# Kernel tuning notes

Measured on AMD Instinct MI355X. Metric: run time of the kernel, lower is better.

Reference implementation:

```python
import jax, jax.numpy as jnp
import numpy as np

B, S, H, D, P = 16, 512, 12, 768, 256
TOP_RATE = 0.1
K = int(round(TOP_RATE * S))  # 51, matches round(self.top_rate * hidden_state.size(1))
LN_EPS = 1e-5


def setup_inputs() -> dict:
    key = jax.random.key(0)
    ks = jax.random.split(key, 6)
    return {
        "hidden_state": jax.random.normal(ks[0], (B, S, D), dtype=jnp.float32),
        "attention": jax.random.normal(ks[1], (B, H, S, S), dtype=jnp.float32),
        "length": S,  # uniform valid length (scalar int)
        # node_trans: Linear(D, P)
        "W_node": jax.random.normal(ks[2], (D, P), dtype=jnp.float32) * 0.02,
        "b_node": jnp.zeros((P,), dtype=jnp.float32),
        # node_eta parameter, initialized to 0 (self.node_eta.data.fill_(0))
        "node_eta": jnp.zeros((1,), dtype=jnp.float32),
        # fc: Linear(P, P)
        "W_fc": jax.random.normal(ks[3], (P, P), dtype=jnp.float32) * 0.02,
        "b_fc": jnp.zeros((P,), dtype=jnp.float32),
        # LayerNorm(P)
        "ln_gamma": jnp.ones((P,), dtype=jnp.float32),
        "ln_beta": jnp.zeros((P,), dtype=jnp.float32),
    }


def reference(hidden_state, attention, W_node, b_node, node_eta, W_fc, b_fc,
              ln_gamma, ln_beta, length):
    # average attention over heads: [B, S, S]
    avg_atten = attention.mean(axis=1)
    # per-target-node top-k neighbors
    vals, idx = jax.lax.top_k(avg_atten, K)  # [B, S, K]
    # edge mask replicating softmax(where(v>0, v, -1e9)) followed by nonzero():
    # entries at -1e9 underflow to exactly 0 in fp32 softmax iff the row has a
    # positive value; otherwise the softmax is uniform and all edges survive.
    keep = vals > 0.0
    row_has_pos = keep.any(axis=-1, keepdims=True)
    keep = jnp.where(row_has_pos, keep, True)            # [B, S, K] (>=1 True per row)
    keepf = keep.astype(hidden_state.dtype)[..., None]   # [B, S, K, 1]

    # node_trans on all nodes: [B, S, P]
    h = hidden_state @ W_node + b_node

    # gather source-node features h[b, idx[b, t, j], :] -> [B, S, K, P]
    gathered = jax.vmap(lambda hb, ib: hb[ib])(h, idx)

    # reduce='mean': edge weight w=1, mailbox mean over kept incoming edges
    h_agg = (gathered * keepf).sum(axis=2) / keepf.sum(axis=2)

    eta = node_eta[0]
    new_h = eta * h + (1.0 - eta) * h_agg                # [B, S, P]

    # dgl.mean_nodes: mean over the `length` nodes of each sub-graph (=S here)
    out = new_h.mean(axis=1)                             # [B, P]

    # fc(dropout(tanh(out))) with dropout in eval mode (identity)
    out = jnp.tanh(out) @ W_fc + b_fc

    # LayerNorm
    mu = out.mean(axis=-1, keepdims=True)
    var = ((out - mu) ** 2).mean(axis=-1, keepdims=True)
    out = (out - mu) / jnp.sqrt(var + LN_EPS) * ln_gamma + ln_beta
    return out
```

## Files before the change

### kernel.cpp

```cpp
#include <hip/hip_runtime.h>
#include <math.h>

#define B_ 16
#define S_ 512
#define H_ 12
#define D_ 768
#define P_ 256
#define K_ 51
#define CH_ 16
#define NCHUNK_ (S_/CH_)

__device__ __forceinline__ unsigned okey(float f) {
  unsigned u = __float_as_uint(f);
  return (u & 0x80000000u) ? ~u : (u | 0x80000000u);
}

__global__ __launch_bounds__(256) void k1_topk_weights(
    const float* __restrict__ attn, float* __restrict__ w) {
  const int bt = blockIdx.x;
  const int b = bt >> 9;
  const int t = bt & (S_ - 1);
  const int tid = threadIdx.x;

  __shared__ unsigned keys[S_];
  __shared__ unsigned hist[256];
  __shared__ unsigned sbuf[256];
  __shared__ int ipar[4];

  const float* base = attn + (((size_t)b * H_) * S_ + t) * S_;
  float2 acc = make_float2(0.f, 0.f);
  #pragma unroll
  for (int h = 0; h < H_; ++h) {
    const float2 v = *(const float2*)(base + (size_t)h * S_ * S_ + 2 * tid);
    acc.x += v.x; acc.y += v.y;
  }
  const float a0 = acc.x * (1.0f / (float)H_);
  const float a1 = acc.y * (1.0f / (float)H_);
  const unsigned k0 = okey(a0);
  const unsigned k1v = okey(a1);
  keys[2 * tid] = k0;
  keys[2 * tid + 1] = k1v;

  if (tid == 0) ipar[0] = 0;
  __syncthreads();
  {
    const int myPos = (a0 > 0.f) + (a1 > 0.f);
    if (myPos) atomicAdd(&ipar[0], myPos);
  }
  __syncthreads();
  const int p = ipar[0];

  bool sel0, sel1;
  float invcnt;
  if (p >= 1 && p < K_) {
    sel0 = (a0 > 0.f);
    sel1 = (a1 > 0.f);
    invcnt = 1.0f / (float)p;
  } else {
    unsigned prefix = 0;
    int remaining = K_;
    #pragma unroll
    for (int pass = 0; pass < 4; ++pass) {
      const int shift = 24 - 8 * pass;
      const unsigned pm = (pass == 0) ? 0u : (0xFFFFFFFFu << (shift + 8));
      hist[tid] = 0;
      __syncthreads();
      if ((k0 & pm) == prefix) atomicAdd(&hist[(k0 >> shift) & 255u], 1u);
      if ((k1v & pm) == prefix) atomicAdd(&hist[(k1v >> shift) & 255u], 1u);
      __syncthreads();
      if (tid < 64) {
        const int lane = tid;
        const unsigned c0 = hist[4 * lane + 0];
        const unsigned c1 = hist[4 * lane + 1];
        const unsigned c2 = hist[4 * lane + 2];
        const unsigned c3 = hist[4 * lane + 3];
        const unsigned loc = c0 + c1 + c2 + c3;
        unsigned suf = loc;
        #pragma unroll
        for (int off = 1; off < 64; off <<= 1) {
          const unsigned v = __shfl_down(suf, off, 64);
          if (lane + off < 64) suf += v;
        }
        const unsigned after = suf - loc;
        sbuf[4 * lane + 3] = after + c3;
        sbuf[4 * lane + 2] = after + c3 + c2;
        sbuf[4 * lane + 1] = after + c3 + c2 + c1;
        sbuf[4 * lane + 0] = after + c3 + c2 + c1 + c0;
      }
      __syncthreads();
      const unsigned sd = sbuf[tid];
      const unsigned sd1 = (tid < 255) ? sbuf[tid + 1] : 0u;
      if (sd >= (unsigned)remaining && sd1 < (unsigned)remaining) {
        ipar[1] = tid;
        ipar[2] = (int)sd1;
        ipar[3] = (int)(sd - sd1);
      }
      __syncthreads();
      prefix |= ((unsigned)ipar[1]) << shift;
      remaining -= ipar[2];
    }
    const unsigned T = prefix;
    const int tieCnt = ipar[3];
    sel0 = (k0 > T);
    sel1 = (k1v > T);
    if (tieCnt == remaining) {
      sel0 |= (k0 == T);
      sel1 |= (k1v == T);
    } else {
      if (k0 == T) {
        int r = 0;
        for (int s2 = 0; s2 < 2 * tid; ++s2) r += (keys[s2] == T);
        if (r < remaining) sel0 = true;
      }
      if (k1v == T) {
        int r = 0;
        for (int s2 = 0; s2 < 2 * tid + 1; ++s2) r += (keys[s2] == T);
        if (r < remaining) sel1 = true;
      }
    }
    invcnt = 1.0f / (float)K_;
  }

  float* wrow = w + b * S_;
  if (sel0) atomicAdd(&wrow[2 * tid], invcnt);
  if (sel1) atomicAdd(&wrow[2 * tid + 1], invcnt);
}

__global__ __launch_bounds__(192) void k2_weighted_sum(
    const float* __restrict__ hidden, const float* __restrict__ w,
    const float* __restrict__ node_eta, float* __restrict__ x) {
  const int chunk = blockIdx.x;
  const int b = blockIdx.y;
  const int tid = threadIdx.x;
  __shared__ float coef[CH_];
  if (tid < CH_) {
    const float eta = node_eta[0];
    const float wv = w[b * S_ + chunk * CH_ + tid];
    coef[tid] = (eta + (1.0f - eta) * wv) * (1.0f / (float)S_);
  }
  __syncthreads();
  const float* hb = hidden + ((size_t)b * S_ + (size_t)chunk * CH_) * D_ + 4 * tid;
  float4 acc = make_float4(0.f, 0.f, 0.f, 0.f);
  #pragma unroll
  for (int s = 0; s < CH_; ++s) {
    const float4 v = *(const float4*)(hb + (size_t)s * D_);
    const float c = coef[s];
    acc.x += c * v.x; acc.y += c * v.y; acc.z += c * v.z; acc.w += c * v.w;
  }
  float* xp = x + b * D_ + 4 * tid;
  atomicAdd(xp + 0, acc.x);
  atomicAdd(xp + 1, acc.y);
  atomicAdd(xp + 2, acc.z);
  atomicAdd(xp + 3, acc.w);
}

__global__ __launch_bounds__(256) void k3_final(
    const float* __restrict__ x, const float* __restrict__ W_node,
    const float* __restrict__ b_node, const float* __restrict__ W_fc,
    const float* __restrict__ b_fc, const float* __restrict__ gamma,
    const float* __restrict__ beta, float* __restrict__ out) {
  const int b = blockIdx.x;
  const int tid = threadIdx.x;
  __shared__ float xs[D_];
  __shared__ float ts[P_];
  __shared__ float red[4];

  for (int d = tid; d < D_; d += 256) xs[d] = x[b * D_ + d];
  __syncthreads();

  float v = b_node[tid];
  for (int d = 0; d < D_; ++d) v += xs[d] * W_node[d * P_ + tid];
  ts[tid] = tanhf(v);
  __syncthreads();

  float o = b_fc[tid];
  for (int q = 0; q < P_; ++q) o += ts[q] * W_fc[q * P_ + tid];

  float s = o;
  #pragma unroll
  for (int off = 32; off > 0; off >>= 1) s += __shfl_down(s, off, 64);
  const int wave = tid >> 6, lane = tid & 63;
  if (lane == 0) red[wave] = s;
  __syncthreads();
  const float mu = (red[0] + red[1] + red[2] + red[3]) * (1.0f / (float)P_);
  __syncthreads();
  const float dv = o - mu;
  float s2 = dv * dv;
  #pragma unroll
  for (int off = 32; off > 0; off >>= 1) s2 += __shfl_down(s2, off, 64);
  if (lane == 0) red[wave] = s2;
  __syncthreads();
  const float var = (red[0] + red[1] + red[2] + red[3]) * (1.0f / (float)P_);
  const float inv = 1.0f / sqrtf(var + 1e-5f);
  out[b * P_ + tid] = dv * inv * gamma[tid] + beta[tid];
}

extern "C" void kernel_launch(void* const* d_in, const int* in_sizes, int n_in,
                              void* d_out, int out_size, void* d_ws, size_t ws_size,
                              hipStream_t stream) {
  (void)in_sizes; (void)n_in; (void)out_size; (void)ws_size;
  const float* hidden   = (const float*)d_in[0];
  const float* attn     = (const float*)d_in[1];
  const float* W_node   = (const float*)d_in[3];
  const float* b_node   = (const float*)d_in[4];
  const float* node_eta = (const float*)d_in[5];
  const float* W_fc     = (const float*)d_in[6];
  const float* b_fc     = (const float*)d_in[7];
  const float* gamma    = (const float*)d_in[8];
  const float* beta     = (const float*)d_in[9];
  float* out = (float*)d_out;

  float* w = (float*)d_ws;
  float* x = w + B_ * S_;
  hipMemsetAsync(d_ws, 0, (size_t)(B_ * S_ + B_ * D_) * sizeof(float), stream);

  k1_topk_weights<<<B_ * S_, 256, 0, stream>>>(attn, w);
  k2_weighted_sum<<<dim3(NCHUNK_, B_), 192, 0, stream>>>(hidden, w, node_eta, x);
  k3_final<<<B_, 256, 0, stream>>>(x, W_node, b_node, W_fc, b_fc, gamma, beta, out);
}
```

Baseline: 362.8 us.

## Streamline radix-select top-k with per-wave histograms, ballot counting, early exit

The radix-select in the top-k kernel now keeps four per-wave histograms, double-buffered so the next pass's clear overlaps the current pass. This removes one barrier per pass and spreads shared-memory atomic contention across waves. The positive-value count uses wave ballots instead of per-thread atomics, the threshold search is folded into the scan wave, and the pass loop exits early once the tie bucket is exactly the remaining count. The final GEMV loops are unrolled. The kernel is likely memory-bound on reading the attention tensor, so the select-path savings may be modest.

```diff
diff --git a/kernel.cpp b/kernel.cpp
--- a/kernel.cpp
+++ b/kernel.cpp
@@ -21,11 +21,14 @@
   const int b = bt >> 9;
   const int t = bt & (S_ - 1);
   const int tid = threadIdx.x;
+  const int wave = tid >> 6;
 
   __shared__ unsigned keys[S_];
-  __shared__ unsigned hist[256];
-  __shared__ unsigned sbuf[256];
+  __shared__ __align__(16) unsigned hist[2][4][256];
   __shared__ int ipar[4];
+
+  ((uint4*)&hist[0][0][0])[tid] = uint4{0u, 0u, 0u, 0u};
+  if (tid == 0) ipar[0] = 0;
 
   const float* base = attn + (((size_t)b * H_) * S_ + t) * S_;
   float2 acc = make_float2(0.f, 0.f);
@@ -41,11 +44,10 @@
   keys[2 * tid] = k0;
   keys[2 * tid + 1] = k1v;
 
-  if (tid == 0) ipar[0] = 0;
-  __syncthreads();
   {
-    const int myPos = (a0 > 0.f) + (a1 > 0.f);
-    if (myPos) atomicAdd(&ipar[0], myPos);
+    const unsigned long long m0 = __ballot(a0 > 0.f);
+    const unsigned long long m1 = __ballot(a1 > 0.f);
+    if ((tid & 63) == 0) atomicAdd(&ipar[0], __popcll(m0) + __popcll(m1));
   }
   __syncthreads();
   const int p = ipar[0];
@@ -59,21 +61,25 @@
   } else {
     unsigned prefix = 0;
     int remaining = K_;
-    #pragma unroll
+    int tieCnt = 0;
+    int exited = 0;
+    unsigned exitm = 0;
     for (int pass = 0; pass < 4; ++pass) {
       const int shift = 24 - 8 * pass;
       const unsigned pm = (pass == 0) ? 0u : (0xFFFFFFFFu << (shift + 8));
-      hist[tid] = 0;
+      const int cur = pass & 1, nxt = cur ^ 1;
+      if ((k0 & pm) == prefix) atomicAdd(&hist[cur][wave][(k0 >> shift) & 255u], 1u);
+      if ((k1v & pm) == prefix) atomicAdd(&hist[cur][wave][(k1v >> shift) & 255u], 1u);
+      ((uint4*)&hist[nxt][0][0])[tid] = uint4{0u, 0u, 0u, 0u};
       __syncthreads();
-      if ((k0 & pm) == prefix) atomicAdd(&hist[(k0 >> shift) & 255u], 1u);
-      if ((k1v & pm) == prefix) atomicAdd(&hist[(k1v >> shift) & 255u], 1u);
-      __syncthreads();
-      if (tid < 64) {
+      if (wave == 0) {
         const int lane = tid;
-        const unsigned c0 = hist[4 * lane + 0];
-        const unsigned c1 = hist[4 * lane + 1];
-        const unsigned c2 = hist[4 * lane + 2];
-        const unsigned c3 = hist[4 * lane + 3];
+        unsigned c0 = 0, c1 = 0, c2 = 0, c3 = 0;
+        #pragma unroll
+        for (int wv = 0; wv < 4; ++wv) {
+          const uint4 v = ((const uint4*)&hist[cur][wv][0])[lane];
+          c0 += v.x; c1 += v.y; c2 += v.z; c3 += v.w;
+        }
         const unsigned loc = c0 + c1 + c2 + c3;
         unsigned suf = loc;
         #pragma unroll
@@ -82,39 +88,42 @@
           if (lane + off < 64) suf += v;
         }
         const unsigned after = suf - loc;
-        sbuf[4 * lane + 3] = after + c3;
-        sbuf[4 * lane + 2] = after + c3 + c2;
-        sbuf[4 * lane + 1] = after + c3 + c2 + c1;
-        sbuf[4 * lane + 0] = after + c3 + c2 + c1 + c0;
+        const unsigned s3 = after + c3;
+        const unsigned s2 = s3 + c2;
+        const unsigned s1 = s2 + c1;
+        const unsigned s0 = s1 + c0;
+        const unsigned rem = (unsigned)remaining;
+        if (s0 >= rem && s1 < rem)    { ipar[1] = 4*lane+0; ipar[2] = (int)s1;    ipar[3] = (int)(s0 - s1); }
+        if (s1 >= rem && s2 < rem)    { ipar[1] = 4*lane+1; ipar[2] = (int)s2;    ipar[3] = (int)(s1 - s2); }
+        if (s2 >= rem && s3 < rem)    { ipar[1] = 4*lane+2; ipar[2] = (int)s3;    ipar[3] = (int)(s2 - s3); }
+        if (s3 >= rem && after < rem) { ipar[1] = 4*lane+3; ipar[2] = (int)after; ipar[3] = (int)(s3 - after); }
       }
       __syncthreads();
-      const unsigned sd = sbuf[tid];
-      const unsigned sd1 = (tid < 255) ? sbuf[tid + 1] : 0u;
-      if (sd >= (unsigned)remaining && sd1 < (unsigned)remaining) {
-        ipar[1] = tid;
-        ipar[2] = (int)sd1;
-        ipar[3] = (int)(sd - sd1);
-      }
-      __syncthreads();
-      prefix |= ((unsigned)ipar[1]) << shift;
+      const int dc = ipar[1];
+      prefix |= ((unsigned)dc) << shift;
       remaining -= ipar[2];
+      tieCnt = ipar[3];
+      if (tieCnt == remaining) {
+        exited = 1;
+        exitm = 0xFFFFFFFFu << shift;
+        break;
+      }
     }
-    const unsigned T = prefix;
-    const int tieCnt = ipar[3];
-    sel0 = (k0 > T);
-    sel1 = (k1v > T);
-    if (tieCnt == remaining) {
-      sel0 |= (k0 == T);
-      sel1 |= (k1v == T);
+    if (exited) {
+      sel0 = (k0 & exitm) >= prefix;
+      sel1 = (k1v & exitm) >= prefix;
     } else {
+      const unsigned T = prefix;
+      sel0 = (k0 > T);
+      sel1 = (k1v > T);
       if (k0 == T) {
         int r = 0;
-        for (int s2 = 0; s2 < 2 * tid; ++s2) r += (keys[s2] == T);
+        for (int s2i = 0; s2i < 2 * tid; ++s2i) r += (keys[s2i] == T);
         if (r < remaining) sel0 = true;
       }
       if (k1v == T) {
         int r = 0;
-        for (int s2 = 0; s2 < 2 * tid + 1; ++s2) r += (keys[s2] == T);
+        for (int s2i = 0; s2i < 2 * tid + 1; ++s2i) r += (keys[s2i] == T);
         if (r < remaining) sel1 = true;
       }
     }
@@ -169,11 +178,13 @@
   __syncthreads();
 
   float v = b_node[tid];
+  #pragma unroll 8
   for (int d = 0; d < D_; ++d) v += xs[d] * W_node[d * P_ + tid];
   ts[tid] = tanhf(v);
   __syncthreads();
 
   float o = b_fc[tid];
+  #pragma unroll 8
   for (int q = 0; q < P_; ++q) o += ts[q] * W_fc[q * P_ + tid];
 
   float s = o;
```

Result: slower. 381.4 us (+5.1%).
